# Kernel tuning notes

Hardware: AMD Instinct MI355X
Metric: run time of the kernel (lower is better)

Reference implementation:

```python
import jax, jax.numpy as jnp
import numpy as np

NEG = -9e15
SLOPE = 0.1  # LeakyReLU negative_slope in the torch module

B, N, NFEAT = 4, 2048, 256
NHID, NHEADS, NOUT = 64, 8, 128


def setup_inputs() -> dict:
    key = jax.random.key(0)
    ks = jax.random.split(key, 8)
    x = jax.random.normal(ks[0], (B, N, NFEAT), dtype=jnp.float32)
    adj = jax.random.randint(ks[1], (B, N, N), 0, 2, dtype=jnp.int32)
    s = 0.1
    Wh = jax.random.normal(ks[2], (NHEADS, NFEAT, NHID), dtype=jnp.float32) * s
    ah = jax.random.normal(ks[3], (NHEADS, 2 * NHID), dtype=jnp.float32) * s
    bh = jax.random.normal(ks[4], (NHEADS, NHID), dtype=jnp.float32) * s
    Wo = jax.random.normal(ks[5], (NHID * NHEADS, NOUT), dtype=jnp.float32) * s
    ao = jax.random.normal(ks[6], (2 * NOUT,), dtype=jnp.float32) * s
    bo = jax.random.normal(ks[7], (NOUT,), dtype=jnp.float32) * s
    return {"x": x, "adj": adj, "Wh": Wh, "ah": ah, "bh": bh,
            "Wo": Wo, "ao": ao, "bo": bo}


def _leaky(v):
    return jnp.where(v >= 0, v, SLOPE * v)


def _gat_layer(x, adj, W, a, b):
    # x: [B,N,Fin], W: [Fin,F], a: [2F], b: [F]
    h = jnp.einsum('bnf,fo->bno', x, W)          # [B,N,F]
    F = W.shape[1]
    a1, a2 = a[:F], a[F:]
    s1 = h @ a1                                   # [B,N] (query / row term)
    s2 = h @ a2                                   # [B,N] (key / col term)
    e = _leaky(s1[:, :, None] + s2[:, None, :])   # [B,N,N], avoids a_input blowup
    e = jnp.where(adj > 0, e, NEG)
    att = jax.nn.softmax(e, axis=2)               # [B,N,N]
    h_prime = jnp.einsum('bnm,bmf->bnf', att, h) + b
    return jax.nn.elu(h_prime)


def reference(x, adj, Wh, ah, bh, Wo, ao, bo):
    # per-head layers, vmapped over the head axis of the stacked params
    heads = jax.vmap(lambda W, a, b: _gat_layer(x, adj, W, a, b))(Wh, ah, bh)
    # [H,B,N,F] -> concat heads along feature dim: [B,N,H*F]
    hcat = jnp.transpose(heads, (1, 2, 0, 3)).reshape(x.shape[0], x.shape[1], -1)
    out = _gat_layer(hcat, adj, Wo, ao, bo)
    return jax.nn.relu(out)
```

## Files before the change

kernel.cpp:

```cpp
#include <hip/hip_runtime.h>

constexpr int B_ = 4;
constexpr int N_ = 2048;
constexpr int NFEAT_ = 256;
constexpr int NHEADS_ = 8;
constexpr float SLOPE_ = 0.1f;
constexpr float L2E = 1.4426950408889634f;

typedef __attribute__((ext_vector_type(8))) __fp16 f16x8;
typedef __attribute__((ext_vector_type(4))) __fp16 f16x4;
typedef __attribute__((ext_vector_type(2))) __fp16 f16x2;
typedef __attribute__((ext_vector_type(4))) float f32x4;

__device__ __forceinline__ f16x8 pack8(const float* v) {
  union { f16x2 h2[4]; f16x8 h8; } u;
  u.h2[0] = __builtin_amdgcn_cvt_pkrtz(v[0], v[1]);
  u.h2[1] = __builtin_amdgcn_cvt_pkrtz(v[2], v[3]);
  u.h2[2] = __builtin_amdgcn_cvt_pkrtz(v[4], v[5]);
  u.h2[3] = __builtin_amdgcn_cvt_pkrtz(v[6], v[7]);
  return u.h8;
}
__device__ __forceinline__ f16x4 pack4(float a, float b, float c, float d) {
  union { f16x2 h2[2]; f16x4 h4; } u;
  u.h2[0] = __builtin_amdgcn_cvt_pkrtz(a, b);
  u.h2[1] = __builtin_amdgcn_cvt_pkrtz(c, d);
  return u.h4;
}

__device__ __forceinline__ unsigned int wmax(f16x2 Ep2, f16x2 Eq2,
                                             unsigned int e1p, unsigned int e2p) {
  f16x2 ea, eb;
  __builtin_memcpy(&ea, &e1p, 4);
  __builtin_memcpy(&eb, &e2p, 4);
  f16x2 a, b, c;
  asm("v_pk_mul_f16 %0, %1, %2" : "=v"(a) : "v"(Ep2), "v"(ea));
  asm("v_pk_mul_f16 %0, %1, %2" : "=v"(b) : "v"(Eq2), "v"(eb));
  asm("v_pk_max_f16 %0, %1, %2" : "=v"(c) : "v"(a), "v"(b));
  unsigned int r;
  __builtin_memcpy(&r, &c, 4);
  return r;
}

__global__ __launch_bounds__(256) void k_prep(
    const int* __restrict__ adj, unsigned short* __restrict__ mask2,
    const float* __restrict__ Wh, __fp16* __restrict__ WhB,
    const float* __restrict__ Wo, __fp16* __restrict__ WoB)
{
  const int bid = blockIdx.x;
  const int l = threadIdx.x & 63;
  if (bid < 4096) {
    const size_t gw = ((size_t)bid * 256 + threadIdx.x) >> 6;
    const int jt = (int)(gw & 31);
    const int ig16 = (int)((gw >> 5) & 127);
    const int b = (int)(gw >> 12);
    const int q = l >> 4, c15 = l & 15;
    const int* base = adj + ((size_t)b * N_ + ig16 * 16) * N_ + jt * 64 + l;
    unsigned int msk = 0;
    #pragma unroll
    for (int r = 0; r < 16; ++r) {
      int a = base[(size_t)r * N_];
      unsigned long long bal = __ballot(a > 0);
      unsigned int v = (unsigned int)((bal >> (q * 8)) & 0xffull)
                     | ((unsigned int)((bal >> (q * 8 + 32)) & 0xffull) << 8);
      if (r == c15) msk = v;
    }
    mask2[gw * 64 + l] = (unsigned short)msk;
  } else if (bid < 4160) {
    int s = (int)(((bid - 4096) * 256 + threadIdx.x) >> 6);
    int h = s >> 5, ks = (s >> 2) & 7, ft = s & 3;
    const float* src = Wh + ((size_t)h * 256 + ks * 32 + (l >> 4) * 8) * 64 + ft * 16 + (l & 15);
    float v[8];
    #pragma unroll
    for (int j = 0; j < 8; ++j) v[j] = src[(size_t)j * 64];
    *(f16x8*)(WhB + (size_t)s * 512 + l * 8) = pack8(v);
  } else {
    int s = (int)(((bid - 4160) * 256 + threadIdx.x) >> 6);
    int ks = s >> 3, ft = s & 7;
    const float* src = Wo + ((size_t)ks * 32 + (l >> 4) * 8) * 128 + ft * 16 + (l & 15);
    float v[8];
    #pragma unroll
    for (int j = 0; j < 8; ++j) v[j] = src[(size_t)j * 128];
    *(f16x8*)(WoB + (size_t)s * 512 + l * 8) = pack8(v);
  }
}

__global__ __launch_bounds__(256, 4) void k_gemm1(
    const float* __restrict__ x, const __fp16* __restrict__ WhB,
    const float* __restrict__ ah,
    __fp16* __restrict__ hB1, float* __restrict__ s1h,
    __fp16* __restrict__ e1h, __fp16* __restrict__ e2h,
    float* __restrict__ pmx1)
{
  constexpr int XP = 264;
  __shared__ __fp16 xs[16 * XP];
  __shared__ __fp16 hT[512 * 16];

  const int t = threadIdx.x;
  const int bid = blockIdx.x;
  const int b = bid >> 7;
  const int n0 = (bid & 127) * 16;

  {
    int r = t >> 4, k0 = (t & 15) * 16;
    const float* src = x + ((size_t)(b * N_) + n0 + r) * NFEAT_ + k0;
    float v0[8], v1[8];
    *(float4*)&v0[0] = *(const float4*)(src);
    *(float4*)&v0[4] = *(const float4*)(src + 4);
    *(float4*)&v1[0] = *(const float4*)(src + 8);
    *(float4*)&v1[4] = *(const float4*)(src + 12);
    *(f16x8*)&xs[r * XP + k0] = pack8(v0);
    *(f16x8*)&xs[r * XP + k0 + 8] = pack8(v1);
  }
  __syncthreads();

  const int w = t >> 6, l = t & 63;
  const int quad = l >> 4, c15 = l & 15;

  f32x4 acc[8];
  #pragma unroll
  for (int i = 0; i < 8; ++i) acc[i] = (f32x4){0.f, 0.f, 0.f, 0.f};

  for (int ks = 0; ks < 8; ++ks) {
    f16x8 af = *(const f16x8*)&xs[c15 * XP + ks * 32 + quad * 8];
    #pragma unroll
    for (int tt = 0; tt < 8; ++tt) {
      int hl = tt >> 2, ft = tt & 3;
      f16x8 bf = *(const f16x8*)(WhB +
          ((((size_t)(2 * w + hl) * 8 + ks) * 4 + ft) * 512) + l * 8);
      acc[tt] = __builtin_amdgcn_mfma_f32_16x16x32_f16(af, bf, acc[tt], 0, 0, 0);
    }
  }

  #pragma unroll
  for (int hl = 0; hl < 2; ++hl) {
    int head = 2 * w + hl;
    float a1v[4], a2v[4];
    #pragma unroll
    for (int ft = 0; ft < 4; ++ft) {
      a1v[ft] = ah[head * 128 + ft * 16 + c15] * L2E;
      a2v[ft] = ah[head * 128 + 64 + ft * 16 + c15] * L2E;
    }
    float hmax = -1e30f;
    #pragma unroll
    for (int r = 0; r < 4; ++r) {
      float v1 = 0.f, v2 = 0.f;
      #pragma unroll
      for (int ft = 0; ft < 4; ++ft) {
        v1 = fmaf(acc[hl * 4 + ft][r], a1v[ft], v1);
        v2 = fmaf(acc[hl * 4 + ft][r], a2v[ft], v2);
      }
      #pragma unroll
      for (int off = 1; off < 16; off <<= 1) {
        v1 += __shfl_xor(v1, off, 64);
        v2 += __shfl_xor(v2, off, 64);
      }
      if (c15 == 0) {
        const size_t nn = (size_t)(b * NHEADS_ + head) * N_ + n0 + quad * 4 + r;
        s1h[nn] = v1;
        e1h[nn] = (__fp16)__builtin_amdgcn_exp2f(v2);
        e2h[nn] = (__fp16)__builtin_amdgcn_exp2f(SLOPE_ * v2);
      }
      hmax = fmaxf(hmax, v2);
    }
    hmax = fmaxf(hmax, __shfl_xor(hmax, 16, 64));
    hmax = fmaxf(hmax, __shfl_xor(hmax, 32, 64));
    if (l == 0)
      pmx1[(size_t)(b * NHEADS_ + head) * 128 + (n0 >> 4)] = hmax;
  }

  #pragma unroll
  for (int tt = 0; tt < 8; ++tt) {
    int f = (2 * w + (tt >> 2)) * 64 + (tt & 3) * 16 + c15;
    *(f16x4*)&hT[f * 16 + quad * 4] =
        pack4(acc[tt][0], acc[tt][1], acc[tt][2], acc[tt][3]);
  }
  __syncthreads();

  const int base_oct = (n0 >> 3) & 3;
  #pragma unroll
  for (int q = 0; q < 4; ++q) {
    int s = t + q * 256;
    int c15v = s & 15, oct = (s >> 4) & 1, ft = (s >> 5) & 3, head = s >> 7;
    f16x8 v = *(const f16x8*)&hT[(head * 64 + ft * 16 + c15v) * 16 + oct * 8];
    int lane0 = (base_oct + oct) * 16 + c15v;
    *(f16x8*)(hB1 +
        ((((size_t)(b * NHEADS_ + head) * 64 + (n0 >> 5)) * 4 + ft) * 512) + lane0 * 8) = v;
  }
}

__global__ __launch_bounds__(256, 4) void k_gemm2(
    const __fp16* __restrict__ g1, const __fp16* __restrict__ WoB,
    const float* __restrict__ ao,
    __fp16* __restrict__ hB2, float* __restrict__ s1o,
    __fp16* __restrict__ e1o, __fp16* __restrict__ e2o,
    float* __restrict__ pmx2)
{
  constexpr int GP = 520;
  __shared__ __fp16 gs[16 * GP];
  __shared__ __fp16 hT[128 * 16];
  __shared__ float sd1[4][16], sd2[4][16];

  const int t = threadIdx.x;
  const int bid = blockIdx.x;
  const int b = bid >> 7;
  const int n0 = (bid & 127) * 16;

  {
    int r = t >> 4, k0 = (t & 15) * 32;
    const __fp16* src = g1 + ((size_t)(b * N_) + n0 + r) * 512 + k0;
    #pragma unroll
    for (int i = 0; i < 4; ++i)
      *(f16x8*)&gs[r * GP + k0 + i * 8] = *(const f16x8*)(src + i * 8);
  }
  __syncthreads();

  const int w = t >> 6, l = t & 63;
  const int quad = l >> 4, c15 = l & 15;

  f32x4 acc[2];
  acc[0] = (f32x4){0.f, 0.f, 0.f, 0.f};
  acc[1] = (f32x4){0.f, 0.f, 0.f, 0.f};

  for (int ks = 0; ks < 16; ++ks) {
    f16x8 af = *(const f16x8*)&gs[c15 * GP + ks * 32 + quad * 8];
    #pragma unroll
    for (int tt = 0; tt < 2; ++tt) {
      int ft = 2 * w + tt;
      f16x8 bf = *(const f16x8*)(WoB + (((size_t)ks * 8 + ft) * 512) + l * 8);
      acc[tt] = __builtin_amdgcn_mfma_f32_16x16x32_f16(af, bf, acc[tt], 0, 0, 0);
    }
  }

  {
    float a1v[2], a2v[2];
    #pragma unroll
    for (int tt = 0; tt < 2; ++tt) {
      int f = (2 * w + tt) * 16 + c15;
      a1v[tt] = ao[f] * L2E;
      a2v[tt] = ao[128 + f] * L2E;
    }
    #pragma unroll
    for (int r = 0; r < 4; ++r) {
      float v1 = acc[0][r] * a1v[0] + acc[1][r] * a1v[1];
      float v2 = acc[0][r] * a2v[0] + acc[1][r] * a2v[1];
      #pragma unroll
      for (int off = 1; off < 16; off <<= 1) {
        v1 += __shfl_xor(v1, off, 64);
        v2 += __shfl_xor(v2, off, 64);
      }
      if (c15 == 0) { sd1[w][quad * 4 + r] = v1; sd2[w][quad * 4 + r] = v2; }
    }
  }

  #pragma unroll
  for (int tt = 0; tt < 2; ++tt) {
    int f = (2 * w + tt) * 16 + c15;
    *(f16x4*)&hT[f * 16 + quad * 4] =
        pack4(acc[tt][0], acc[tt][1], acc[tt][2], acc[tt][3]);
  }
  __syncthreads();

  if (t < 16)
    s1o[(size_t)b * N_ + n0 + t] = sd1[0][t] + sd1[1][t] + sd1[2][t] + sd1[3][t];
  else if (t < 32) {
    int rr = t - 16;
    float v = sd2[0][rr] + sd2[1][rr] + sd2[2][rr] + sd2[3][rr];
    e1o[(size_t)b * N_ + n0 + rr] = (__fp16)__builtin_amdgcn_exp2f(v);
    e2o[(size_t)b * N_ + n0 + rr] = (__fp16)__builtin_amdgcn_exp2f(SLOPE_ * v);
    float hm = v;
    hm = fmaxf(hm, __shfl_xor(hm, 1, 64));
    hm = fmaxf(hm, __shfl_xor(hm, 2, 64));
    hm = fmaxf(hm, __shfl_xor(hm, 4, 64));
    hm = fmaxf(hm, __shfl_xor(hm, 8, 64));
    if (rr == 0) pmx2[(size_t)b * 128 + (n0 >> 4)] = hm;
  }

  {
    int c15v = t & 15, oct = (t >> 4) & 1, ft = t >> 5;
    f16x8 v = *(const f16x8*)&hT[(ft * 16 + c15v) * 16 + oct * 8];
    int base_oct = (n0 >> 3) & 3;
    int lane0 = (base_oct + oct) * 16 + c15v;
    *(f16x8*)(hB2 +
        (((size_t)(b * 64 + (n0 >> 5)) * 8 + ft) * 512) + lane0 * 8) = v;
  }
}

__global__ __launch_bounds__(512, 4) void k_att1(
    const __fp16* __restrict__ hB, const float* __restrict__ s1,
    const __fp16* __restrict__ e1, const __fp16* __restrict__ e2,
    const float* __restrict__ pmx1,
    const unsigned short* __restrict__ mask2,
    const float* __restrict__ bias, __fp16* __restrict__ g1)
{
  constexpr int NRG = 4, NJQ = 2, JLEN = 1024, TJ = 64, NIT = JLEN / TJ;
  constexpr int TILE = TJ * 64;

  __shared__ __fp16 vbuf[NJQ][2][TILE];
  __shared__ __fp16 ets[2][N_];
  __shared__ uint2 mlut[16];

  const int tid = threadIdx.x;
  const int w = tid >> 6, l = tid & 63;
  const int quad = l >> 4, c15 = l & 15;
  const int rowg = w % NRG, jq = w / NRG;
  const int tc = rowg * 64 + l;

  int idx = blockIdx.x;
  const int ig = idx & 31; idx >>= 5;
  const int head = idx & 7;
  const int b = idx >> 3;
  const int i0w = ig * 64 + rowg * 16;
  const int bh = b * NHEADS_ + head;

  const float* s1p = s1 + (size_t)bh * N_;
  const char* hBp = (const char*)(hB + (size_t)bh * (N_ / 32) * 2048);
  const unsigned short* mp = mask2 + ((size_t)(b * 128 + (i0w >> 4)) * 32) * 64 + l;

  const int jbase = jq * JLEN;

  if (tid < 16) {
    unsigned int v = tid;
    mlut[tid] = (uint2){ ((v & 1u) ? 0xffffu : 0u) | ((v & 2u) ? 0xffff0000u : 0u),
                         ((v & 4u) ? 0xffffu : 0u) | ((v & 8u) ? 0xffff0000u : 0u) };
  }

  float4 pA0 = *(const float4*)(hBp + (size_t)(jbase >> 5) * 4096 + tc * 16);
  float4 pA1 = *(const float4*)(hBp + (size_t)(jbase >> 5) * 4096 + (tc + 256) * 16);
  float4 pB0 = *(const float4*)(hBp + (size_t)((jbase + TJ) >> 5) * 4096 + tc * 16);
  float4 pB1 = *(const float4*)(hBp + (size_t)((jbase + TJ) >> 5) * 4096 + (tc + 256) * 16);
  unsigned short mk = mp[(size_t)(jbase >> 6) * 64];

  {
    const int half = tid >> 8, off = (tid & 255) * 8;
    const __fp16* src = (half ? e2 : e1) + (size_t)bh * N_ + off;
    *(f16x8*)&ets[half][off] = *(const f16x8*)src;
  }

  const float s1v = s1p[i0w + c15];
  float s2m;
  {
    const float* pm = pmx1 + (size_t)bh * 128;
    float tmx = fmaxf(pm[l], pm[l + 64]);
    #pragma unroll
    for (int off = 1; off < 64; off <<= 1)
      tmx = fmaxf(tmx, __shfl_xor(tmx, off, 64));
    s2m = tmx;
  }
  *(float4*)((char*)&vbuf[jq][0][0] + tc * 16) = pA0;
  *(float4*)((char*)&vbuf[jq][0][0] + (tc + 256) * 16) = pA1;
  __syncthreads();

  const float zm = s1v + s2m;
  const float m = fmaxf(zm, SLOPE_ * zm);
  const float Ep = __builtin_amdgcn_exp2f(s1v - m);
  const float Eq = __builtin_amdgcn_exp2f(SLOPE_ * s1v - m);
  const f16x2 Ep2 = __builtin_amdgcn_cvt_pkrtz(Ep, Ep);
  const f16x2 Eq2 = __builtin_amdgcn_cvt_pkrtz(Eq, Eq);

  f16x8 ones;
  #pragma unroll
  for (int i = 0; i < 8; ++i) ones[i] = (__fp16)1.0f;

  f32x4 acc[4], acc5;
  #pragma unroll
  for (int t = 0; t < 4; ++t) acc[t] = (f32x4){0.f, 0.f, 0.f, 0.f};
  acc5 = (f32x4){0.f, 0.f, 0.f, 0.f};

  for (int it = 0; it < NIT; ++it) {
    const int cur = it & 1;
    const int j0 = jbase + it * TJ;
    if (it + 1 < NIT) {
      *(float4*)((char*)&vbuf[jq][cur ^ 1][0] + tc * 16) = pB0;
      *(float4*)((char*)&vbuf[jq][cur ^ 1][0] + (tc + 256) * 16) = pB1;
    }
    if (it + 2 < NIT) {
      pB0 = *(const float4*)(hBp + (size_t)((j0 + 2 * TJ) >> 5) * 4096 + tc * 16);
      pB1 = *(const float4*)(hBp + (size_t)((j0 + 2 * TJ) >> 5) * 4096 + (tc + 256) * 16);
    }
    unsigned short nk = 0;
    if (it + 1 < NIT) nk = mp[(size_t)((j0 + TJ) >> 6) * 64];

    #pragma unroll
    for (int h = 0; h < 2; ++h) {
      const int jk = j0 + h * 32;
      uint4 e1u = *(const uint4*)((const char*)&ets[0][jk] + quad * 16);
      uint4 e2u = *(const uint4*)((const char*)&ets[1][jk] + quad * 16);
      const unsigned int mbyte = ((unsigned int)mk >> (8 * h)) & 0xffu;
      const uint2 mA = mlut[mbyte & 15u];
      const uint2 mB = mlut[mbyte >> 4];
      union { unsigned int u[4]; f16x8 v8; } af;
      af.u[0] = wmax(Ep2, Eq2, e1u.x, e2u.x) & mA.x;
      af.u[1] = wmax(Ep2, Eq2, e1u.y, e2u.y) & mA.y;
      af.u[2] = wmax(Ep2, Eq2, e1u.z, e2u.z) & mB.x;
      af.u[3] = wmax(Ep2, Eq2, e1u.w, e2u.w) & mB.y;
      const f16x8 a = af.v8;
      acc5 = __builtin_amdgcn_mfma_f32_16x16x32_f16(a, ones, acc5, 0, 0, 0);
      const __fp16* vb = &vbuf[jq][cur][h * 2048];
      #pragma unroll
      for (int t = 0; t < 4; ++t) {
        f16x8 bf = *(const f16x8*)(vb + t * 512 + l * 8);
        acc[t] = __builtin_amdgcn_mfma_f32_16x16x32_f16(a, bf, acc[t], 0, 0, 0);
      }
    }
    mk = nk;
    __syncthreads();
  }

  auto pacc = (float(*)[16][64])(&vbuf[0][0][0]);
  auto pls  = (float(*)[16])((char*)&vbuf[0][0][0] + 16384);
  if (jq == 1) {
    #pragma unroll
    for (int t = 0; t < 4; ++t)
      #pragma unroll
      for (int r = 0; r < 4; ++r)
        pacc[rowg][quad * 4 + r][t * 16 + c15] = acc[t][r];
    if (c15 == 0) {
      #pragma unroll
      for (int r = 0; r < 4; ++r) pls[rowg][quad * 4 + r] = acc5[r];
    }
  }
  __syncthreads();
  if (jq == 0) {
    float Lrow[4];
    #pragma unroll
    for (int r = 0; r < 4; ++r)
      Lrow[r] = acc5[r] + pls[rowg][quad * 4 + r];
    #pragma unroll
    for (int t = 0; t < 4; ++t)
      #pragma unroll
      for (int r = 0; r < 4; ++r)
        acc[t][r] += pacc[rowg][quad * 4 + r][t * 16 + c15];
    float lr[4];
    #pragma unroll
    for (int r = 0; r < 4; ++r) lr[r] = 1.f / Lrow[r];
    #pragma unroll
    for (int t = 0; t < 4; ++t) {
      const float bv = bias[head * 64 + t * 16 + c15];
      #pragma unroll
      for (int r = 0; r < 4; ++r) {
        const int i = i0w + quad * 4 + r;
        float v = acc[t][r] * lr[r] + bv;
        v = (v > 0.f) ? v : expm1f(v);
        g1[(size_t)(b * N_ + i) * 512 + head * 64 + t * 16 + c15] = (__fp16)v;
      }
    }
  }
}

__global__ __launch_bounds__(512, 4) void k_att2(
    const __fp16* __restrict__ hB, const float* __restrict__ s1,
    const __fp16* __restrict__ e1, const __fp16* __restrict__ e2,
    const float* __restrict__ pmx2,
    const unsigned short* __restrict__ mask2,
    const float* __restrict__ bias, float* __restrict__ out)
{
  constexpr int NRG = 2, NJQ = 4, JLEN = 512, TJ = 32, NIT = JLEN / TJ;
  constexpr int TILE = TJ * 64;

  __shared__ __fp16 vbuf[NJQ][2][TILE];
  __shared__ __fp16 ets[2][N_];
  __shared__ uint2 mlut[16];

  const int tid = threadIdx.x;
  const int w = tid >> 6, l = tid & 63;
  const int quad = l >> 4, c15 = l & 15;
  const int rowg = w % NRG, jq = w / NRG;
  const int tc = rowg * 64 + l;

  int idx = blockIdx.x;
  const int ig = idx & 63; idx >>= 6;
  const int fs = idx & 1;
  const int b = idx >> 1;
  const int i0w = ig * 32 + rowg * 16;

  const float* s1p = s1 + (size_t)b * N_;
  const char* hBp = (const char*)(hB + (size_t)b * 64 * 4096 + fs * 2048);
  const unsigned short* mp = mask2 + ((size_t)(b * 128 + (i0w >> 4)) * 32) * 64 + l;

  const int jbase = jq * JLEN;

  if (tid < 16) {
    unsigned int v = tid;
    mlut[tid] = (uint2){ ((v & 1u) ? 0xffffu : 0u) | ((v & 2u) ? 0xffff0000u : 0u),
                         ((v & 4u) ? 0xffffu : 0u) | ((v & 8u) ? 0xffff0000u : 0u) };
  }

  float4 pA0 = *(const float4*)(hBp + (size_t)(jbase >> 5) * 8192 + tc * 16);
  float4 pA1 = *(const float4*)(hBp + (size_t)(jbase >> 5) * 8192 + (tc + 128) * 16);
  float4 pB0 = *(const float4*)(hBp + (size_t)((jbase + TJ) >> 5) * 8192 + tc * 16);
  float4 pB1 = *(const float4*)(hBp + (size_t)((jbase + TJ) >> 5) * 8192 + (tc + 128) * 16);
  unsigned short mk = mp[(size_t)(jbase >> 6) * 64];

  {
    const int half = tid >> 8, off = (tid & 255) * 8;
    const __fp16* src = (half ? e2 : e1) + (size_t)b * N_ + off;
    *(f16x8*)&ets[half][off] = *(const f16x8*)src;
  }

  const float s1v = s1p[i0w + c15];
  float s2m;
  {
    const float* pm = pmx2 + (size_t)b * 128;
    float tmx = fmaxf(pm[l], pm[l + 64]);
    #pragma unroll
    for (int off = 1; off < 64; off <<= 1)
      tmx = fmaxf(tmx, __shfl_xor(tmx, off, 64));
    s2m = tmx;
  }
  *(float4*)((char*)&vbuf[jq][0][0] + tc * 16) = pA0;
  *(float4*)((char*)&vbuf[jq][0][0] + (tc + 128) * 16) = pA1;
  __syncthreads();

  const float zm = s1v + s2m;
  const float m = fmaxf(zm, SLOPE_ * zm);
  const float Ep = __builtin_amdgcn_exp2f(s1v - m);
  const float Eq = __builtin_amdgcn_exp2f(SLOPE_ * s1v - m);
  const f16x2 Ep2 = __builtin_amdgcn_cvt_pkrtz(Ep, Ep);
  const f16x2 Eq2 = __builtin_amdgcn_cvt_pkrtz(Eq, Eq);

  f16x8 ones;
  #pragma unroll
  for (int i = 0; i < 8; ++i) ones[i] = (__fp16)1.0f;

  f32x4 acc[4], acc5;
  #pragma unroll
  for (int t = 0; t < 4; ++t) acc[t] = (f32x4){0.f, 0.f, 0.f, 0.f};
  acc5 = (f32x4){0.f, 0.f, 0.f, 0.f};

  for (int it = 0; it < NIT; ++it) {
    const int cur = it & 1;
    const int j0 = jbase + it * TJ;
    if (it + 1 < NIT) {
      *(float4*)((char*)&vbuf[jq][cur ^ 1][0] + tc * 16) = pB0;
      *(float4*)((char*)&vbuf[jq][cur ^ 1][0] + (tc + 128) * 16) = pB1;
    }
    if (it + 2 < NIT) {
      pB0 = *(const float4*)(hBp + (size_t)((j0 + 2 * TJ) >> 5) * 8192 + tc * 16);
      pB1 = *(const float4*)(hBp + (size_t)((j0 + 2 * TJ) >> 5) * 8192 + (tc + 128) * 16);
    }
    unsigned short nk = 0;
    if (it + 1 < NIT) nk = mp[(size_t)((j0 + TJ) >> 6) * 64];

    uint4 e1u = *(const uint4*)((const char*)&ets[0][j0] + quad * 16);
    uint4 e2u = *(const uint4*)((const char*)&ets[1][j0] + quad * 16);
    const unsigned int mbyte = ((unsigned int)mk >> (8 * ((j0 >> 5) & 1))) & 0xffu;
    const uint2 mA = mlut[mbyte & 15u];
    const uint2 mB = mlut[mbyte >> 4];
    union { unsigned int u[4]; f16x8 v8; } af;
    af.u[0] = wmax(Ep2, Eq2, e1u.x, e2u.x) & mA.x;
    af.u[1] = wmax(Ep2, Eq2, e1u.y, e2u.y) & mA.y;
    af.u[2] = wmax(Ep2, Eq2, e1u.z, e2u.z) & mB.x;
    af.u[3] = wmax(Ep2, Eq2, e1u.w, e2u.w) & mB.y;
    const f16x8 a = af.v8;
    acc5 = __builtin_amdgcn_mfma_f32_16x16x32_f16(a, ones, acc5, 0, 0, 0);
    const __fp16* vb = &vbuf[jq][cur][0];
    #pragma unroll
    for (int t = 0; t < 4; ++t) {
      f16x8 bf = *(const f16x8*)(vb + t * 512 + l * 8);
      acc[t] = __builtin_amdgcn_mfma_f32_16x16x32_f16(a, bf, acc[t], 0, 0, 0);
    }
    mk = nk;
    __syncthreads();
  }

  auto pacc = (float(*)[NRG][16][64])(&vbuf[0][0][0]);
  auto pls  = (float(*)[NRG][16])((char*)&vbuf[0][0][0] + 24576);
  if (jq > 0) {
    #pragma unroll
    for (int t = 0; t < 4; ++t)
      #pragma unroll
      for (int r = 0; r < 4; ++r)
        pacc[jq - 1][rowg][quad * 4 + r][t * 16 + c15] = acc[t][r];
    if (c15 == 0) {
      #pragma unroll
      for (int r = 0; r < 4; ++r) pls[jq - 1][rowg][quad * 4 + r] = acc5[r];
    }
  }
  __syncthreads();
  if (jq == 0) {
    float Lrow[4];
    #pragma unroll
    for (int r = 0; r < 4; ++r) Lrow[r] = acc5[r];
    #pragma unroll
    for (int q = 0; q < NJQ - 1; ++q) {
      #pragma unroll
      for (int t = 0; t < 4; ++t)
        #pragma unroll
        for (int r = 0; r < 4; ++r)
          acc[t][r] += pacc[q][rowg][quad * 4 + r][t * 16 + c15];
      #pragma unroll
      for (int r = 0; r < 4; ++r) Lrow[r] += pls[q][rowg][quad * 4 + r];
    }
    float lr[4];
    #pragma unroll
    for (int r = 0; r < 4; ++r) lr[r] = 1.f / Lrow[r];
    #pragma unroll
    for (int t = 0; t < 4; ++t) {
      const float bv = bias[fs * 64 + t * 16 + c15];
      #pragma unroll
      for (int r = 0; r < 4; ++r) {
        const int i = i0w + quad * 4 + r;
        float v = acc[t][r] * lr[r] + bv;
        out[(size_t)(b * N_ + i) * 128 + fs * 64 + t * 16 + c15] = fmaxf(v, 0.f);
      }
    }
  }
}

extern "C" void kernel_launch(void* const* d_in, const int* in_sizes, int n_in,
                              void* d_out, int out_size, void* d_ws, size_t ws_size,
                              hipStream_t stream) {
  const float* x   = (const float*)d_in[0];
  const int*   adj = (const int*)d_in[1];
  const float* Wh  = (const float*)d_in[2];
  const float* ah  = (const float*)d_in[3];
  const float* bh  = (const float*)d_in[4];
  const float* Wo  = (const float*)d_in[5];
  const float* ao  = (const float*)d_in[6];
  const float* bo  = (const float*)d_in[7];
  float* out = (float*)d_out;

  float* ws   = (float*)d_ws;
  float* s1h  = ws;
  float* s2h  = s1h  + (size_t)B_ * NHEADS_ * N_;
  float* s1o  = s2h  + (size_t)B_ * NHEADS_ * N_;
  float* s2o  = s1o  + (size_t)B_ * N_;
  __fp16* g1  = (__fp16*)(s2o + (size_t)B_ * N_);
  __fp16* hB1 = g1  + (size_t)B_ * N_ * 512;
  __fp16* hB2 = hB1 + (size_t)B_ * NHEADS_ * N_ * 64;
  __fp16* WhB = hB2 + (size_t)B_ * N_ * 128;
  __fp16* WoB = WhB + (size_t)8 * 256 * 64;
  unsigned short* mask2 = (unsigned short*)(WoB + (size_t)512 * 128);
  __fp16* e1h = (__fp16*)(mask2 + (size_t)B_ * 128 * 32 * 64);
  __fp16* e2h = e1h + (size_t)B_ * NHEADS_ * N_;
  __fp16* e1o = e2h + (size_t)B_ * NHEADS_ * N_;
  __fp16* e2o = e1o + (size_t)B_ * N_;
  float* pmx1 = (float*)(e2o + (size_t)B_ * N_);
  float* pmx2 = pmx1 + (size_t)B_ * NHEADS_ * 128;

  k_prep<<<4192, 256, 0, stream>>>(adj, mask2, Wh, WhB, Wo, WoB);
  k_gemm1<<<B_ * (N_ / 16), 256, 0, stream>>>(x, WhB, ah, hB1, s1h, e1h, e2h, pmx1);
  k_att1<<<B_ * NHEADS_ * (N_ / 64), 512, 0, stream>>>(
      hB1, s1h, e1h, e2h, pmx1, mask2, bh, g1);
  k_gemm2<<<B_ * (N_ / 16), 256, 0, stream>>>(g1, WoB, ao, hB2, s1o, e1o, e2o, pmx2);
  k_att2<<<B_ * 2 * (N_ / 32), 512, 0, stream>>>(
      hB2, s1o, e1o, e2o, pmx2, mask2, bo, out);
}
```

Measured before the change: 184.3 us.

## Restructure k_att1 so each wave owns distinct rows over full key range

```diff
diff --git a/kernel.cpp b/kernel.cpp
--- a/kernel.cpp
+++ b/kernel.cpp
@@ -292,31 +292,27 @@
     const unsigned short* __restrict__ mask2,
     const float* __restrict__ bias, __fp16* __restrict__ g1)
 {
-  constexpr int NRG = 4, NJQ = 2, JLEN = 1024, TJ = 64, NIT = JLEN / TJ;
+  constexpr int TJ = 128, NIT = N_ / TJ;
   constexpr int TILE = TJ * 64;
 
-  __shared__ __fp16 vbuf[NJQ][2][TILE];
+  __shared__ __fp16 vbuf[2][TILE];
   __shared__ __fp16 ets[2][N_];
   __shared__ uint2 mlut[16];
 
   const int tid = threadIdx.x;
   const int w = tid >> 6, l = tid & 63;
   const int quad = l >> 4, c15 = l & 15;
-  const int rowg = w % NRG, jq = w / NRG;
-  const int tc = rowg * 64 + l;
 
   int idx = blockIdx.x;
-  const int ig = idx & 31; idx >>= 5;
+  const int ig = idx & 15; idx >>= 4;
   const int head = idx & 7;
   const int b = idx >> 3;
-  const int i0w = ig * 64 + rowg * 16;
+  const int i0w = ig * 128 + w * 16;
   const int bh = b * NHEADS_ + head;
 
   const float* s1p = s1 + (size_t)bh * N_;
   const char* hBp = (const char*)(hB + (size_t)bh * (N_ / 32) * 2048);
   const unsigned short* mp = mask2 + ((size_t)(b * 128 + (i0w >> 4)) * 32) * 64 + l;
-
-  const int jbase = jq * JLEN;
 
   if (tid < 16) {
     unsigned int v = tid;
@@ -324,11 +320,12 @@
                          ((v & 4u) ? 0xffffu : 0u) | ((v & 8u) ? 0xffff0000u : 0u) };
   }
 
-  float4 pA0 = *(const float4*)(hBp + (size_t)(jbase >> 5) * 4096 + tc * 16);
-  float4 pA1 = *(const float4*)(hBp + (size_t)(jbase >> 5) * 4096 + (tc + 256) * 16);
-  float4 pB0 = *(const float4*)(hBp + (size_t)((jbase + TJ) >> 5) * 4096 + tc * 16);
-  float4 pB1 = *(const float4*)(hBp + (size_t)((jbase + TJ) >> 5) * 4096 + (tc + 256) * 16);
-  unsigned short mk = mp[(size_t)(jbase >> 6) * 64];
+  float4 pA0 = *(const float4*)(hBp + tid * 16);
+  float4 pA1 = *(const float4*)(hBp + 8192 + tid * 16);
+  float4 pB0 = *(const float4*)(hBp + 16384 + tid * 16);
+  float4 pB1 = *(const float4*)(hBp + 16384 + 8192 + tid * 16);
+  unsigned short mk0 = mp[0];
+  unsigned short mk1 = mp[64];
 
   {
     const int half = tid >> 8, off = (tid & 255) * 8;
@@ -346,8 +343,8 @@
       tmx = fmaxf(tmx, __shfl_xor(tmx, off, 64));
     s2m = tmx;
   }
-  *(float4*)((char*)&vbuf[jq][0][0] + tc * 16) = pA0;
-  *(float4*)((char*)&vbuf[jq][0][0] + (tc + 256) * 16) = pA1;
+  *(float4*)((char*)&vbuf[0][0] + tid * 16) = pA0;
+  *(float4*)((char*)&vbuf[0][0] + 8192 + tid * 16) = pA1;
   __syncthreads();
 
   const float zm = s1v + s2m;
@@ -368,24 +365,28 @@
 
   for (int it = 0; it < NIT; ++it) {
     const int cur = it & 1;
-    const int j0 = jbase + it * TJ;
     if (it + 1 < NIT) {
-      *(float4*)((char*)&vbuf[jq][cur ^ 1][0] + tc * 16) = pB0;
-      *(float4*)((char*)&vbuf[jq][cur ^ 1][0] + (tc + 256) * 16) = pB1;
+      *(float4*)((char*)&vbuf[cur ^ 1][0] + tid * 16) = pB0;
+      *(float4*)((char*)&vbuf[cur ^ 1][0] + 8192 + tid * 16) = pB1;
     }
     if (it + 2 < NIT) {
-      pB0 = *(const float4*)(hBp + (size_t)((j0 + 2 * TJ) >> 5) * 4096 + tc * 16);
-      pB1 = *(const float4*)(hBp + (size_t)((j0 + 2 * TJ) >> 5) * 4096 + (tc + 256) * 16);
-    }
-    unsigned short nk = 0;
-    if (it + 1 < NIT) nk = mp[(size_t)((j0 + TJ) >> 6) * 64];
-
-    #pragma unroll
-    for (int h = 0; h < 2; ++h) {
-      const int jk = j0 + h * 32;
+      const char* srcb = hBp + (size_t)(it + 2) * 16384;
+      pB0 = *(const float4*)(srcb + tid * 16);
+      pB1 = *(const float4*)(srcb + 8192 + tid * 16);
+    }
+    unsigned short nk0 = 0, nk1 = 0;
+    if (it + 1 < NIT) {
+      nk0 = mp[(size_t)(it + 1) * 128];
+      nk1 = mp[(size_t)(it + 1) * 128 + 64];
+    }
+
+    #pragma unroll
+    for (int h = 0; h < 4; ++h) {
+      const int jk = it * TJ + h * 32;
       uint4 e1u = *(const uint4*)((const char*)&ets[0][jk] + quad * 16);
       uint4 e2u = *(const uint4*)((const char*)&ets[1][jk] + quad * 16);
-      const unsigned int mbyte = ((unsigned int)mk >> (8 * h)) & 0xffu;
+      const unsigned int mword = (h < 2) ? (unsigned int)mk0 : (unsigned int)mk1;
+      const unsigned int mbyte = (mword >> (8 * (h & 1))) & 0xffu;
       const uint2 mA = mlut[mbyte & 15u];
       const uint2 mB = mlut[mbyte >> 4];
       union { unsigned int u[4]; f16x8 v8; } af;
@@ -395,54 +396,29 @@
       af.u[3] = wmax(Ep2, Eq2, e1u.w, e2u.w) & mB.y;
       const f16x8 a = af.v8;
       acc5 = __builtin_amdgcn_mfma_f32_16x16x32_f16(a, ones, acc5, 0, 0, 0);
-      const __fp16* vb = &vbuf[jq][cur][h * 2048];
+      const __fp16* vb = &vbuf[cur][h * 2048];
       #pragma unroll
       for (int t = 0; t < 4; ++t) {
         f16x8 bf = *(const f16x8*)(vb + t * 512 + l * 8);
         acc[t] = __builtin_amdgcn_mfma_f32_16x16x32_f16(a, bf, acc[t], 0, 0, 0);
       }
     }
-    mk = nk;
+    mk0 = nk0; mk1 = nk1;
     __syncthreads();
   }
 
-  auto pacc = (float(*)[16][64])(&vbuf[0][0][0]);
-  auto pls  = (float(*)[16])((char*)&vbuf[0][0][0] + 16384);
-  if (jq == 1) {
-    #pragma unroll
-    for (int t = 0; t < 4; ++t)
-      #pragma unroll
-      for (int r = 0; r < 4; ++r)
-        pacc[rowg][quad * 4 + r][t * 16 + c15] = acc[t][r];
-    if (c15 == 0) {
-      #pragma unroll
-      for (int r = 0; r < 4; ++r) pls[rowg][quad * 4 + r] = acc5[r];
-    }
-  }
-  __syncthreads();
-  if (jq == 0) {
-    float Lrow[4];
-    #pragma unroll
-    for (int r = 0; r < 4; ++r)
-      Lrow[r] = acc5[r] + pls[rowg][quad * 4 + r];
-    #pragma unroll
-    for (int t = 0; t < 4; ++t)
-      #pragma unroll
-      for (int r = 0; r < 4; ++r)
-        acc[t][r] += pacc[rowg][quad * 4 + r][t * 16 + c15];
-    float lr[4];
-    #pragma unroll
-    for (int r = 0; r < 4; ++r) lr[r] = 1.f / Lrow[r];
-    #pragma unroll
-    for (int t = 0; t < 4; ++t) {
-      const float bv = bias[head * 64 + t * 16 + c15];
-      #pragma unroll
-      for (int r = 0; r < 4; ++r) {
-        const int i = i0w + quad * 4 + r;
-        float v = acc[t][r] * lr[r] + bv;
-        v = (v > 0.f) ? v : expm1f(v);
-        g1[(size_t)(b * N_ + i) * 512 + head * 64 + t * 16 + c15] = (__fp16)v;
-      }
+  float lr[4];
+  #pragma unroll
+  for (int r = 0; r < 4; ++r) lr[r] = 1.f / acc5[r];
+  #pragma unroll
+  for (int t = 0; t < 4; ++t) {
+    const float bv = bias[head * 64 + t * 16 + c15];
+    #pragma unroll
+    for (int r = 0; r < 4; ++r) {
+      const int i = i0w + quad * 4 + r;
+      float v = acc[t][r] * lr[r] + bv;
+      v = (v > 0.f) ? v : expm1f(v);
+      g1[(size_t)(b * N_ + i) * 512 + head * 64 + t * 16 + c15] = (__fp16)v;
     }
   }
 }
@@ -640,7 +616,7 @@
 
   k_prep<<<4192, 256, 0, stream>>>(adj, mask2, Wh, WhB, Wo, WoB);
   k_gemm1<<<B_ * (N_ / 16), 256, 0, stream>>>(x, WhB, ah, hB1, s1h, e1h, e2h, pmx1);
-  k_att1<<<B_ * NHEADS_ * (N_ / 64), 512, 0, stream>>>(
+  k_att1<<<B_ * NHEADS_ * (N_ / 128), 512, 0, stream>>>(
       hB1, s1h, e1h, e2h, pmx1, mask2, bh, g1);
   k_gemm2<<<B_ * (N_ / 16), 256, 0, stream>>>(g1, WoB, ao, hB2, s1o, e1o, e2o, pmx2);
   k_att2<<<B_ * 2 * (N_ / 32), 512, 0, stream>>>(
```

New measurement: 176.0 us (median of 2 runs). 1.05x faster.
